# Performance work log

Hardware: AMD Instinct MI355X
Metric: run time of the kernel (lower is better)

The kernel has to match this reference:

```python
import jax, jax.numpy as jnp
import numpy as np
from jax import lax

EPS = 1e-5
C4 = 192   # embed_dim // 4
ED = 768   # embed_dim


def _conv(x, w, stride, pad):
    return lax.conv_general_dilated(x, w, (stride, stride), pad,
                                    dimension_numbers=('NCHW', 'OIHW', 'NCHW'))


def _bn(x, g, b, m, v):
    # inference-mode batchnorm over channel dim (NCHW)
    inv = g * lax.rsqrt(v + EPS)
    return x * inv[None, :, None, None] + (b - m * inv)[None, :, None, None]


def _gelu(x):
    return jax.nn.gelu(x, approximate=False)  # torch nn.GELU default = exact erf


def _region(x, w, g, b, m, v, grid):
    # x: (B,C,H,W); w: (G,C,C,3,3); bn params: (G,C); G = gh*gw
    B, C, H, W = x.shape
    gh, gw = grid
    th, tw = H // gh, W // gw
    tiles = x.reshape(B, C, gh, th, gw, tw).transpose(2, 4, 0, 1, 3, 5)
    tiles = tiles.reshape(gh * gw, B, C, th, tw)

    def per_tile(t, wi, gi, bi, mi, vi):
        y = _gelu(_bn(_conv(t, wi, 1, 'SAME'), gi, bi, mi, vi))
        return y + t  # residual

    out = jax.vmap(per_tile)(tiles, w, g, b, m, v)  # (G,B,C,th,tw)
    out = out.reshape(gh, gw, B, C, th, tw).transpose(2, 3, 0, 4, 1, 5)
    return out.reshape(B, C, H, W)


def _bn_params(key, c):
    k1, k2, k3, k4 = jax.random.split(key, 4)
    return (1.0 + 0.1 * jax.random.normal(k1, (c,)),
            0.1 * jax.random.normal(k2, (c,)),
            0.1 * jax.random.normal(k3, (c,)),
            jax.random.uniform(k4, (c,), minval=0.5, maxval=1.5))


def setup_inputs() -> dict:
    key = jax.random.key(0)
    ks = jax.random.split(key, 12)
    x = jax.random.normal(ks[0], (64, 3, 224, 224), dtype=jnp.float32)
    conv1_w = 0.02 * jax.random.normal(ks[1], (C4, 3, 4, 4))
    bn1_g, bn1_b, bn1_m, bn1_v = _bn_params(ks[2], C4)
    r1_w = 0.02 * jax.random.normal(ks[3], (64, C4, C4, 3, 3))
    r1_g, r1_b, r1_m, r1_v = _bn_params(ks[4], C4)
    r1_g, r1_b, r1_m, r1_v = (jnp.tile(p[None], (64, 1)) * (1.0 + 0.01 * jax.random.normal(jax.random.fold_in(ks[4], i), (64, C4))) for i, p in enumerate((r1_g, r1_b, r1_m, r1_v)))
    conv2_w = 0.02 * jax.random.normal(ks[5], (C4, C4, 2, 2))
    bn2_g, bn2_b, bn2_m, bn2_v = _bn_params(ks[6], C4)
    r2_w = 0.02 * jax.random.normal(ks[7], (16, C4, C4, 3, 3))
    r2_g, r2_b, r2_m, r2_v = _bn_params(ks[8], C4)
    r2_g, r2_b, r2_m, r2_v = (jnp.tile(p[None], (16, 1)) * (1.0 + 0.01 * jax.random.normal(jax.random.fold_in(ks[8], i), (16, C4))) for i, p in enumerate((r2_g, r2_b, r2_m, r2_v)))
    conv3_w = 0.02 * jax.random.normal(ks[9], (ED, C4, 2, 2))
    bn3_g, bn3_b, bn3_m, bn3_v = _bn_params(ks[10], ED)
    return dict(x=x, conv1_w=conv1_w, bn1_g=bn1_g, bn1_b=bn1_b, bn1_m=bn1_m, bn1_v=bn1_v,
                r1_w=r1_w, r1_g=r1_g, r1_b=r1_b, r1_m=r1_m, r1_v=r1_v,
                conv2_w=conv2_w, bn2_g=bn2_g, bn2_b=bn2_b, bn2_m=bn2_m, bn2_v=bn2_v,
                r2_w=r2_w, r2_g=r2_g, r2_b=r2_b, r2_m=r2_m, r2_v=r2_v,
                conv3_w=conv3_w, bn3_g=bn3_g, bn3_b=bn3_b, bn3_m=bn3_m, bn3_v=bn3_v)


def reference(x, conv1_w, bn1_g, bn1_b, bn1_m, bn1_v,
              r1_w, r1_g, r1_b, r1_m, r1_v,
              conv2_w, bn2_g, bn2_b, bn2_m, bn2_v,
              r2_w, r2_g, r2_b, r2_m, r2_v,
              conv3_w, bn3_g, bn3_b, bn3_m, bn3_v):
    h = _gelu(_bn(_conv(x, conv1_w, 4, 'VALID'), bn1_g, bn1_b, bn1_m, bn1_v))   # (B,192,56,56)
    h = _region(h, r1_w, r1_g, r1_b, r1_m, r1_v, (8, 8))
    h = _gelu(_bn(_conv(h, conv2_w, 2, 'VALID'), bn2_g, bn2_b, bn2_m, bn2_v))   # (B,192,28,28)
    h = _region(h, r2_w, r2_g, r2_b, r2_m, r2_v, (4, 4))
    h = _bn(_conv(h, conv3_w, 2, 'VALID'), bn3_g, bn3_b, bn3_m, bn3_v)          # (B,768,14,14)
    B = h.shape[0]
    return h.reshape(B, ED, -1).transpose(0, 2, 1)                               # (B,196,768)
```

## Files before the change

kernel.cpp:

```cpp
#include <hip/hip_runtime.h>
#include <hip/hip_bf16.h>
#include <math.h>

#define EPSBN 1e-5f

typedef short short8 __attribute__((ext_vector_type(8)));
typedef short short4v __attribute__((ext_vector_type(4)));
typedef float floatx4 __attribute__((ext_vector_type(4)));

__device__ __forceinline__ float gelu_f(float x) {
    return 0.5f * x * (1.0f + erff(x * 0.70710678118654752f));
}

__device__ __forceinline__ unsigned short f2bf(float f) {
    union { float f; unsigned int u; } c; c.f = f;
    unsigned int u = c.u;
    unsigned int r = (u + 0x7FFFu + ((u >> 16) & 1u)) >> 16;
    return (unsigned short)r;
}

__device__ __forceinline__ float bf2f(unsigned short h) {
    union { unsigned int u; float f; } c; c.u = ((unsigned int)h) << 16;
    return c.f;
}

__global__ void wprep_bf16_k(const float* __restrict__ w, unsigned short* __restrict__ wb,
                             long total) {
    for (long o = (long)blockIdx.x * blockDim.x + threadIdx.x; o < total;
         o += (long)gridDim.x * blockDim.x) {
        int ic = (int)(o % 192); long t0 = o / 192;
        int t = (int)(t0 % 9); long t1 = t0 / 9;
        int oc = (int)(t1 % 192); long g = t1 / 192;
        wb[o] = f2bf(w[(((size_t)g * 192 + oc) * 192 + ic) * 9 + t]);
    }
}

__global__ void wprep_tap_k(const float* __restrict__ w, unsigned short* __restrict__ wb,
                            int OC) {
    long total = (long)4 * OC * 192;
    for (long o = (long)blockIdx.x * blockDim.x + threadIdx.x; o < total;
         o += (long)gridDim.x * blockDim.x) {
        int ic = (int)(o % 192); long t0 = o / 192;
        int oc = (int)(t0 % OC); int t = (int)(t0 / OC);
        wb[o] = f2bf(w[((size_t)oc * 192 + ic) * 4 + t]);
    }
}

__global__ void wprep_wt1_k(const float* __restrict__ w, float* __restrict__ wt) {
    int o = blockIdx.x * 256 + threadIdx.x;
    if (o < 9216) {
        int oc = o % 192, k = o / 192;
        wt[o] = w[oc * 48 + k];
    }
}

__global__ __launch_bounds__(192) void conv1_k(
        const float* __restrict__ x, const float* __restrict__ wt1,
        const float* __restrict__ bg, const float* __restrict__ bb,
        const float* __restrict__ bm, const float* __restrict__ bv,
        unsigned short* __restrict__ h1c) {
    __shared__ float xs[3][4][224];
    int b = blockIdx.x / 56, oy = blockIdx.x % 56;
    int tid = threadIdx.x;
    for (int i = tid; i < 2688; i += 192) {
        int col = i % 224, r = (i / 224) % 4, c = i / 896;
        xs[c][r][col] = x[(((size_t)b * 3 + c) * 224 + 4 * oy + r) * 224 + col];
    }
    float w[48];
    #pragma unroll
    for (int k = 0; k < 48; k++) w[k] = wt1[k * 192 + tid];
    float inv = bg[tid] * rsqrtf(bv[tid] + EPSBN);
    float bet = bb[tid] - bm[tid] * inv;
    __syncthreads();
    for (int ox = 0; ox < 56; ox++) {
        float a = 0.f;
        #pragma unroll
        for (int c = 0; c < 3; c++) {
            #pragma unroll
            for (int ky = 0; ky < 4; ky++) {
                float4 v = *(const float4*)&xs[c][ky][4 * ox];
                const float* wk = &w[(c * 4 + ky) * 4];
                a += v.x * wk[0] + v.y * wk[1] + v.z * wk[2] + v.w * wk[3];
            }
        }
        h1c[(((size_t)b * 56 + oy) * 56 + ox) * 192 + tid] = f2bf(gelu_f(a * inv + bet));
    }
}

#define RST 200
#define TILE_SH (81 * RST)
template<int INF32>
__global__ __launch_bounds__(256, 2) void region_mfma3_k(
        const void* __restrict__ inbuf, void* __restrict__ outbuf,
        const unsigned short* __restrict__ wb,
        const float* __restrict__ pg, const float* __restrict__ pb,
        const float* __restrict__ pm, const float* __restrict__ pv,
        int gw, int W) {
    __shared__ unsigned short lds[2 * TILE_SH];
    const int raw = blockIdx.x;
    const int g = (raw & 7) + 8 * (raw >> 8);
    const int bp = (raw >> 3) & 31;
    const int b0 = bp * 2;
    const int gy = g / gw, gx = g % gw;
    const int Y0 = gy * 7, X0 = gx * 7;
    const int tid = threadIdx.x;
    const int lane = tid & 63;
    const int wid = tid >> 6;
    const int quad = lane >> 4;
    const int l15 = lane & 15;

    const size_t tsz = (size_t)W * W * 192;
    const size_t slab0 = (size_t)b0 * tsz;

    for (int i = tid; i < 1536; i += 256) {
        int tI = i / 768, rem = i % 768, h = rem / 24, ch = rem % 24;
        int cell;
        if (h < 9) cell = h;
        else if (h < 18) cell = 72 + (h - 9);
        else { int h2 = h - 18; cell = (1 + (h2 >> 1)) * 9 + ((h2 & 1) * 8); }
        *(short8*)&lds[tI * TILE_SH + cell * RST + ch * 8] = (short8)0;
    }
    for (int i = tid; i < 2352; i += 256) {
        int tI = i / 1176, rem = i % 1176, p = rem / 24, ch = rem % 24;
        int y = p / 7, xx = p % 7;
        size_t poff = slab0 + (size_t)tI * tsz + ((size_t)(Y0 + y) * W + (X0 + xx)) * 192 + ch * 8;
        short8 v;
        if (INF32) {
            const float* s4 = (const float*)inbuf + poff;
            float4 a = *(const float4*)s4;
            float4 b2 = *(const float4*)(s4 + 4);
            v[0] = (short)f2bf(a.x);  v[1] = (short)f2bf(a.y);
            v[2] = (short)f2bf(a.z);  v[3] = (short)f2bf(a.w);
            v[4] = (short)f2bf(b2.x); v[5] = (short)f2bf(b2.y);
            v[6] = (short)f2bf(b2.z); v[7] = (short)f2bf(b2.w);
        } else {
            v = *(const short8*)((const unsigned short*)inbuf + poff);
        }
        *(short8*)&lds[tI * TILE_SH + ((y + 1) * 9 + (xx + 1)) * RST + ch * 8] = v;
    }
    __syncthreads();

    int pyv[4], pxv[4];
    #pragma unroll
    for (int f = 0; f < 4; f++) {
        int p = f * 16 + l15; if (p > 48) p = 48;
        pyv[f] = p / 7; pxv[f] = p % 7;
    }
    int woff[3];
    #pragma unroll
    for (int nt = 0; nt < 3; nt++)
        woff[nt] = (wid * 48 + nt * 16 + l15) * 1728 + quad * 8;
    const unsigned short* wbg = wb + (size_t)g * 331776;

    floatx4 acc[8][3];
    #pragma unroll
    for (int m = 0; m < 8; m++)
        #pragma unroll
        for (int nt = 0; nt < 3; nt++) acc[m][nt] = (floatx4)0.f;

    for (int t = 0; t < 9; t++) {
        const int ky = t / 3, kx = t % 3;
        int ca[8];
        #pragma unroll
        for (int f = 0; f < 4; f++) {
            int cell = ((pyv[f] + ky) * 9 + (pxv[f] + kx)) * RST + quad * 8;
            ca[f] = cell;
            ca[4 + f] = TILE_SH + cell;
        }
        const int toff = t * 192;
        #pragma unroll
        for (int s = 0; s < 6; s++) {
            const int ic0 = s * 32;
            short8 wf[3];
            #pragma unroll
            for (int nt = 0; nt < 3; nt++)
                wf[nt] = *(const short8*)(wbg + woff[nt] + toff + ic0);
            short8 pf[8];
            #pragma unroll
            for (int m = 0; m < 8; m++)
                pf[m] = *(const short8*)&lds[ca[m] + ic0];
            #pragma unroll
            for (int m = 0; m < 8; m++)
                #pragma unroll
                for (int nt = 0; nt < 3; nt++)
                    acc[m][nt] = __builtin_amdgcn_mfma_f32_16x16x32_bf16(pf[m], wf[nt], acc[m][nt], 0, 0, 0);
        }
    }

    #pragma unroll
    for (int nt = 0; nt < 3; nt++) {
        int oc = wid * 48 + nt * 16 + l15;
        float inv = pg[g * 192 + oc] * rsqrtf(pv[g * 192 + oc] + EPSBN);
        float bet = pb[g * 192 + oc] - pm[g * 192 + oc] * inv;
        #pragma unroll
        for (int m = 0; m < 8; m++) {
            const int tI = m >> 3 ? 1 : (m >> 2);
            const int f = m & 3;
            const size_t tslab = slab0 + (size_t)tI * tsz;
            unsigned short* outb = (unsigned short*)outbuf + tslab;
            const float* resf = (const float*)inbuf + tslab;
            const unsigned short* resu = (const unsigned short*)inbuf + tslab;
            #pragma unroll
            for (int r = 0; r < 4; r++) {
                int p = f * 16 + quad * 4 + r;
                if (p < 49) {
                    int y = p / 7, xx = p % 7;
                    size_t pix = (size_t)(Y0 + y) * W + (X0 + xx);
                    float res = INF32 ? resf[pix * 192 + oc] : bf2f(resu[pix * 192 + oc]);
                    outb[pix * 192 + oc] = f2bf(gelu_f(acc[m][nt][r] * inv + bet) + res);
                }
            }
        }
    }
}

__global__ __launch_bounds__(256) void conv2_mfma_k(
        const unsigned short* __restrict__ h1c, const unsigned short* __restrict__ wb,
        const float* __restrict__ bg, const float* __restrict__ bb,
        const float* __restrict__ bm, const float* __restrict__ bv,
        float* __restrict__ h2c) {
    __shared__ unsigned short lds[2 * 112 * 40];
    const int b = blockIdx.x / 7;
    const int oy0 = (blockIdx.x % 7) * 4;
    const int tid = threadIdx.x;
    const int lane = tid & 63;
    const int wid = tid >> 6;
    const int quad = lane >> 4;
    const int l15 = lane & 15;

    floatx4 acc[7][3];
    #pragma unroll
    for (int mt = 0; mt < 7; mt++)
        #pragma unroll
        for (int nt = 0; nt < 3; nt++) acc[mt][nt] = (floatx4)0.f;

    for (int ky = 0; ky < 2; ky++) {
        for (int c = 0; c < 6; c++) {
            __syncthreads();
            for (int i = tid; i < 1792; i += 256) {
                int icq = i & 7, kx = (i >> 3) & 1, p = i >> 4;
                int oy = oy0 + p / 28, ox = p % 28;
                int iy = 2 * oy + ky, ix = 2 * ox + kx;
                const unsigned short* src =
                    h1c + (((size_t)b * 56 + iy) * 56 + ix) * 192 + c * 32 + icq * 4;
                *(short4v*)(&lds[kx * 4480 + p * 40 + icq * 4]) = *(const short4v*)src;
            }
            __syncthreads();
            #pragma unroll
            for (int kx = 0; kx < 2; kx++) {
                const int t = ky * 2 + kx;
                short8 wf[3];
                #pragma unroll
                for (int nt = 0; nt < 3; nt++) {
                    int oc = wid * 48 + nt * 16 + l15;
                    wf[nt] = *(const short8*)(wb + ((size_t)(t * 192 + oc)) * 192 + c * 32 + quad * 8);
                }
                #pragma unroll
                for (int mt = 0; mt < 7; mt++) {
                    short8 ap = *(const short8*)(&lds[kx * 4480 + (mt * 16 + l15) * 40 + quad * 8]);
                    #pragma unroll
                    for (int nt = 0; nt < 3; nt++)
                        acc[mt][nt] = __builtin_amdgcn_mfma_f32_16x16x32_bf16(ap, wf[nt], acc[mt][nt], 0, 0, 0);
                }
            }
        }
    }
    #pragma unroll
    for (int nt = 0; nt < 3; nt++) {
        int oc = wid * 48 + nt * 16 + l15;
        float inv = bg[oc] * rsqrtf(bv[oc] + EPSBN);
        float bet = bb[oc] - bm[oc] * inv;
        #pragma unroll
        for (int mt = 0; mt < 7; mt++) {
            #pragma unroll
            for (int r = 0; r < 4; r++) {
                int p = mt * 16 + quad * 4 + r;
                int oy = oy0 + p / 28, ox = p % 28;
                h2c[(((size_t)b * 28 + oy) * 28 + ox) * 192 + oc] = gelu_f(acc[mt][nt][r] * inv + bet);
            }
        }
    }
}

__global__ __launch_bounds__(256) void conv3_mfma_k(
        const unsigned short* __restrict__ h2b, const unsigned short* __restrict__ wb,
        const float* __restrict__ bg, const float* __restrict__ bb,
        const float* __restrict__ bm, const float* __restrict__ bv,
        float* __restrict__ out) {
    __shared__ unsigned short lds[2 * 112 * 40];
    const int bid = blockIdx.x;
    const int b = bid / 6;
    const int s = (bid % 6) / 3;
    const int octile = bid % 3;
    const int y0 = s * 7;
    const int tid = threadIdx.x;
    const int lane = tid & 63;
    const int wid = tid >> 6;
    const int quad = lane >> 4;
    const int l15 = lane & 15;

    floatx4 acc[7][4];
    #pragma unroll
    for (int mt = 0; mt < 7; mt++)
        #pragma unroll
        for (int nt = 0; nt < 4; nt++) acc[mt][nt] = (floatx4)0.f;

    for (int ky = 0; ky < 2; ky++) {
        for (int c = 0; c < 6; c++) {
            __syncthreads();
            for (int i = tid; i < 1568; i += 256) {
                int icq = i & 7, kx = (i >> 3) & 1, p = i >> 4;
                int oy = y0 + p / 14, ox = p % 14;
                int iy = 2 * oy + ky, ix = 2 * ox + kx;
                const unsigned short* src =
                    h2b + (((size_t)b * 28 + iy) * 28 + ix) * 192 + c * 32 + icq * 4;
                *(short4v*)(&lds[kx * 4480 + p * 40 + icq * 4]) = *(const short4v*)src;
            }
            __syncthreads();
            #pragma unroll
            for (int kx = 0; kx < 2; kx++) {
                const int t = ky * 2 + kx;
                short8 wf[4];
                #pragma unroll
                for (int nt = 0; nt < 4; nt++) {
                    int oc = octile * 256 + wid * 64 + nt * 16 + l15;
                    wf[nt] = *(const short8*)(wb + ((size_t)(t * 768 + oc)) * 192 + c * 32 + quad * 8);
                }
                #pragma unroll
                for (int mt = 0; mt < 7; mt++) {
                    int p = mt * 16 + l15; if (p > 97) p = 97;
                    short8 ap = *(const short8*)(&lds[kx * 4480 + p * 40 + quad * 8]);
                    #pragma unroll
                    for (int nt = 0; nt < 4; nt++)
                        acc[mt][nt] = __builtin_amdgcn_mfma_f32_16x16x32_bf16(ap, wf[nt], acc[mt][nt], 0, 0, 0);
                }
            }
        }
    }
    #pragma unroll
    for (int nt = 0; nt < 4; nt++) {
        int oc = octile * 256 + wid * 64 + nt * 16 + l15;
        float inv = bg[oc] * rsqrtf(bv[oc] + EPSBN);
        float bet = bb[oc] - bm[oc] * inv;
        #pragma unroll
        for (int mt = 0; mt < 7; mt++) {
            #pragma unroll
            for (int r = 0; r < 4; r++) {
                int p = mt * 16 + quad * 4 + r;
                if (p < 98) {
                    int oy = y0 + p / 14, ox = p % 14;
                    out[((size_t)b * 196 + oy * 14 + ox) * 768 + oc] = acc[mt][nt][r] * inv + bet;
                }
            }
        }
    }
}

extern "C" void kernel_launch(void* const* d_in, const int* in_sizes, int n_in,
                              void* d_out, int out_size, void* d_ws, size_t ws_size,
                              hipStream_t stream) {
    const float* x   = (const float*)d_in[0];
    const float* w1  = (const float*)d_in[1];
    const float* b1g = (const float*)d_in[2];
    const float* b1b = (const float*)d_in[3];
    const float* b1m = (const float*)d_in[4];
    const float* b1v = (const float*)d_in[5];
    const float* r1w = (const float*)d_in[6];
    const float* r1g = (const float*)d_in[7];
    const float* r1b = (const float*)d_in[8];
    const float* r1m = (const float*)d_in[9];
    const float* r1v = (const float*)d_in[10];
    const float* w2  = (const float*)d_in[11];
    const float* b2g = (const float*)d_in[12];
    const float* b2b = (const float*)d_in[13];
    const float* b2m = (const float*)d_in[14];
    const float* b2v = (const float*)d_in[15];
    const float* r2w = (const float*)d_in[16];
    const float* r2g = (const float*)d_in[17];
    const float* r2b = (const float*)d_in[18];
    const float* r2m = (const float*)d_in[19];
    const float* r2v = (const float*)d_in[20];
    const float* w3  = (const float*)d_in[21];
    const float* b3g = (const float*)d_in[22];
    const float* b3b = (const float*)d_in[23];
    const float* b3m = (const float*)d_in[24];
    const float* b3v = (const float*)d_in[25];
    float* out = (float*)d_out;

    char* ws = (char*)d_ws;
    unsigned short* h1c  = (unsigned short*)(ws + 0);
    float*          h2c  = (float*)         (ws + 77070336UL);
    unsigned short* h2b  = (unsigned short*)(ws + 115605504UL);
    unsigned short* wb1  = (unsigned short*)(ws + 134873088UL);
    unsigned short* wb2r = (unsigned short*)(ws + 177340416UL);
    float*          wt1  = (float*)         (ws + 187957248UL);
    unsigned short* wb2c = (unsigned short*)(ws + 187994112UL);
    unsigned short* wb3c = (unsigned short*)(ws + 188289024UL);

    wprep_bf16_k<<<8192, 256, 0, stream>>>(r1w, wb1, (long)64 * 192 * 9 * 192);
    wprep_bf16_k<<<2048, 256, 0, stream>>>(r2w, wb2r, (long)16 * 192 * 9 * 192);
    wprep_tap_k<<<576, 256, 0, stream>>>(w2, wb2c, 192);
    wprep_tap_k<<<2304, 256, 0, stream>>>(w3, wb3c, 768);
    wprep_wt1_k<<<36, 256, 0, stream>>>(w1, wt1);

    conv1_k<<<64 * 56, 192, 0, stream>>>(x, wt1, b1g, b1b, b1m, b1v, h1c);
    region_mfma3_k<0><<<64 * 32, 256, 0, stream>>>(h1c, h1c, wb1, r1g, r1b, r1m, r1v, 8, 56);
    conv2_mfma_k<<<64 * 7, 256, 0, stream>>>(h1c, wb2c, b2g, b2b, b2m, b2v, h2c);
    region_mfma3_k<1><<<16 * 32, 256, 0, stream>>>(h2c, h2b, wb2r, r2g, r2b, r2m, r2v, 4, 28);
    conv3_mfma_k<<<64 * 6, 256, 0, stream>>>(h2b, wb3c, b3g, b3b, b3m, b3v, out);
}
```

Measured before the change: 867.4 us.

## Split conv1 rows, compact region LDS tile, load conv2/conv3 operands directly

conv1 now launches two blocks per output row, each covering half the columns, which doubles the grid and halves per-block work. The region kernel drops the padded 9x9 halo layout for a compact 7x7 tile plus one zero cell, and maps out-of-range taps to that cell; this shrinks LDS use and the zeroing work. conv2 and conv3 drop their LDS staging and __syncthreads, loading MFMA A-fragments straight from global memory with precomputed pixel offsets and fully unrolled loops. This removes the barriers and staging copies, at the cost of uncoalesced global loads and higher register pressure.

After: 873.3 us. Within noise of the previous version (+0.7%).

```diff
diff --git a/kernel.cpp b/kernel.cpp
--- a/kernel.cpp
+++ b/kernel.cpp
@@ -5,7 +5,6 @@
 #define EPSBN 1e-5f
 
 typedef short short8 __attribute__((ext_vector_type(8)));
-typedef short short4v __attribute__((ext_vector_type(4)));
 typedef float floatx4 __attribute__((ext_vector_type(4)));
 
 __device__ __forceinline__ float gelu_f(float x) {
@@ -59,12 +58,15 @@
         const float* __restrict__ bg, const float* __restrict__ bb,
         const float* __restrict__ bm, const float* __restrict__ bv,
         unsigned short* __restrict__ h1c) {
-    __shared__ float xs[3][4][224];
-    int b = blockIdx.x / 56, oy = blockIdx.x % 56;
+    __shared__ float xs[3][4][112];
+    int b = blockIdx.x / 112;
+    int rest = blockIdx.x % 112;
+    int oy = rest >> 1;
+    int ox0 = (rest & 1) * 28;
     int tid = threadIdx.x;
-    for (int i = tid; i < 2688; i += 192) {
-        int col = i % 224, r = (i / 224) % 4, c = i / 896;
-        xs[c][r][col] = x[(((size_t)b * 3 + c) * 224 + 4 * oy + r) * 224 + col];
+    for (int i = tid; i < 1344; i += 192) {
+        int col = i % 112, r = (i / 112) % 4, c = i / 448;
+        xs[c][r][col] = x[(((size_t)b * 3 + c) * 224 + 4 * oy + r) * 224 + 4 * ox0 + col];
     }
     float w[48];
     #pragma unroll
@@ -72,7 +74,7 @@
     float inv = bg[tid] * rsqrtf(bv[tid] + EPSBN);
     float bet = bb[tid] - bm[tid] * inv;
     __syncthreads();
-    for (int ox = 0; ox < 56; ox++) {
+    for (int ox = 0; ox < 28; ox++) {
         float a = 0.f;
         #pragma unroll
         for (int c = 0; c < 3; c++) {
@@ -83,14 +85,15 @@
                 a += v.x * wk[0] + v.y * wk[1] + v.z * wk[2] + v.w * wk[3];
             }
         }
-        h1c[(((size_t)b * 56 + oy) * 56 + ox) * 192 + tid] = f2bf(gelu_f(a * inv + bet));
+        h1c[(((size_t)b * 56 + oy) * 56 + (ox0 + ox)) * 192 + tid] = f2bf(gelu_f(a * inv + bet));
     }
 }
 
 #define RST 200
-#define TILE_SH (81 * RST)
+#define NCELL 50
+#define TILE_SH (NCELL * RST)
 template<int INF32>
-__global__ __launch_bounds__(256, 2) void region_mfma3_k(
+__global__ __launch_bounds__(256, 2) void region_mfma4_k(
         const void* __restrict__ inbuf, void* __restrict__ outbuf,
         const unsigned short* __restrict__ wb,
         const float* __restrict__ pg, const float* __restrict__ pb,
@@ -112,13 +115,9 @@
     const size_t tsz = (size_t)W * W * 192;
     const size_t slab0 = (size_t)b0 * tsz;
 
-    for (int i = tid; i < 1536; i += 256) {
-        int tI = i / 768, rem = i % 768, h = rem / 24, ch = rem % 24;
-        int cell;
-        if (h < 9) cell = h;
-        else if (h < 18) cell = 72 + (h - 9);
-        else { int h2 = h - 18; cell = (1 + (h2 >> 1)) * 9 + ((h2 & 1) * 8); }
-        *(short8*)&lds[tI * TILE_SH + cell * RST + ch * 8] = (short8)0;
+    for (int i = tid; i < 48; i += 256) {
+        int tI = i / 24, ch = i % 24;
+        *(short8*)&lds[tI * TILE_SH + 49 * RST + ch * 8] = (short8)0;
     }
     for (int i = tid; i < 2352; i += 256) {
         int tI = i / 1176, rem = i % 1176, p = rem / 24, ch = rem % 24;
@@ -136,7 +135,7 @@
         } else {
             v = *(const short8*)((const unsigned short*)inbuf + poff);
         }
-        *(short8*)&lds[tI * TILE_SH + ((y + 1) * 9 + (xx + 1)) * RST + ch * 8] = v;
+        *(short8*)&lds[tI * TILE_SH + p * RST + ch * 8] = v;
     }
     __syncthreads();
 
@@ -158,14 +157,17 @@
         #pragma unroll
         for (int nt = 0; nt < 3; nt++) acc[m][nt] = (floatx4)0.f;
 
+    #pragma unroll
     for (int t = 0; t < 9; t++) {
-        const int ky = t / 3, kx = t % 3;
+        const int dy = t / 3 - 1, dx = t % 3 - 1;
         int ca[8];
         #pragma unroll
         for (int f = 0; f < 4; f++) {
-            int cell = ((pyv[f] + ky) * 9 + (pxv[f] + kx)) * RST + quad * 8;
-            ca[f] = cell;
-            ca[4 + f] = TILE_SH + cell;
+            int yy = pyv[f] + dy, xx2 = pxv[f] + dx;
+            bool ok = ((unsigned)yy < 7u) & ((unsigned)xx2 < 7u);
+            int cell = ok ? (yy * 7 + xx2) : 49;
+            ca[f] = cell * RST + quad * 8;
+            ca[4 + f] = TILE_SH + ca[f];
         }
         const int toff = t * 192;
         #pragma unroll
@@ -194,7 +196,7 @@
         float bet = pb[g * 192 + oc] - pm[g * 192 + oc] * inv;
         #pragma unroll
         for (int m = 0; m < 8; m++) {
-            const int tI = m >> 3 ? 1 : (m >> 2);
+            const int tI = m >> 2;
             const int f = m & 3;
             const size_t tslab = slab0 + (size_t)tI * tsz;
             unsigned short* outb = (unsigned short*)outbuf + tslab;
@@ -219,7 +221,6 @@
         const float* __restrict__ bg, const float* __restrict__ bb,
         const float* __restrict__ bm, const float* __restrict__ bv,
         float* __restrict__ h2c) {
-    __shared__ unsigned short lds[2 * 112 * 40];
     const int b = blockIdx.x / 7;
     const int oy0 = (blockIdx.x % 7) * 4;
     const int tid = threadIdx.x;
@@ -228,40 +229,43 @@
     const int quad = lane >> 4;
     const int l15 = lane & 15;
 
+    size_t pixoff[7];
+    #pragma unroll
+    for (int mt = 0; mt < 7; mt++) {
+        int p = mt * 16 + l15;
+        int oy = oy0 + p / 28, ox = p % 28;
+        pixoff[mt] = (((size_t)b * 56 + 2 * oy) * 56 + 2 * ox) * 192 + quad * 8;
+    }
+
     floatx4 acc[7][3];
     #pragma unroll
     for (int mt = 0; mt < 7; mt++)
         #pragma unroll
         for (int nt = 0; nt < 3; nt++) acc[mt][nt] = (floatx4)0.f;
 
+    #pragma unroll
     for (int ky = 0; ky < 2; ky++) {
-        for (int c = 0; c < 6; c++) {
-            __syncthreads();
-            for (int i = tid; i < 1792; i += 256) {
-                int icq = i & 7, kx = (i >> 3) & 1, p = i >> 4;
-                int oy = oy0 + p / 28, ox = p % 28;
-                int iy = 2 * oy + ky, ix = 2 * ox + kx;
-                const unsigned short* src =
-                    h1c + (((size_t)b * 56 + iy) * 56 + ix) * 192 + c * 32 + icq * 4;
-                *(short4v*)(&lds[kx * 4480 + p * 40 + icq * 4]) = *(const short4v*)src;
-            }
-            __syncthreads();
-            #pragma unroll
-            for (int kx = 0; kx < 2; kx++) {
-                const int t = ky * 2 + kx;
+        #pragma unroll
+        for (int kx = 0; kx < 2; kx++) {
+            const int t = ky * 2 + kx;
+            const size_t aoff = ((size_t)ky * 56 + kx) * 192;
+            #pragma unroll
+            for (int c = 0; c < 6; c++) {
                 short8 wf[3];
                 #pragma unroll
                 for (int nt = 0; nt < 3; nt++) {
                     int oc = wid * 48 + nt * 16 + l15;
                     wf[nt] = *(const short8*)(wb + ((size_t)(t * 192 + oc)) * 192 + c * 32 + quad * 8);
                 }
-                #pragma unroll
-                for (int mt = 0; mt < 7; mt++) {
-                    short8 ap = *(const short8*)(&lds[kx * 4480 + (mt * 16 + l15) * 40 + quad * 8]);
+                short8 ap[7];
+                #pragma unroll
+                for (int mt = 0; mt < 7; mt++)
+                    ap[mt] = *(const short8*)(h1c + pixoff[mt] + aoff + c * 32);
+                #pragma unroll
+                for (int mt = 0; mt < 7; mt++)
                     #pragma unroll
                     for (int nt = 0; nt < 3; nt++)
-                        acc[mt][nt] = __builtin_amdgcn_mfma_f32_16x16x32_bf16(ap, wf[nt], acc[mt][nt], 0, 0, 0);
-                }
+                        acc[mt][nt] = __builtin_amdgcn_mfma_f32_16x16x32_bf16(ap[mt], wf[nt], acc[mt][nt], 0, 0, 0);
             }
         }
     }
@@ -287,7 +291,6 @@
         const float* __restrict__ bg, const float* __restrict__ bb,
         const float* __restrict__ bm, const float* __restrict__ bv,
         float* __restrict__ out) {
-    __shared__ unsigned short lds[2 * 112 * 40];
     const int bid = blockIdx.x;
     const int b = bid / 6;
     const int s = (bid % 6) / 3;
@@ -299,41 +302,43 @@
     const int quad = lane >> 4;
     const int l15 = lane & 15;
 
+    size_t pixoff[7];
+    #pragma unroll
+    for (int mt = 0; mt < 7; mt++) {
+        int p = mt * 16 + l15; if (p > 97) p = 97;
+        int oy = y0 + p / 14, ox = p % 14;
+        pixoff[mt] = (((size_t)b * 28 + 2 * oy) * 28 + 2 * ox) * 192 + quad * 8;
+    }
+
     floatx4 acc[7][4];
     #pragma unroll
     for (int mt = 0; mt < 7; mt++)
         #pragma unroll
         for (int nt = 0; nt < 4; nt++) acc[mt][nt] = (floatx4)0.f;
 
+    #pragma unroll
     for (int ky = 0; ky < 2; ky++) {
-        for (int c = 0; c < 6; c++) {
-            __syncthreads();
-            for (int i = tid; i < 1568; i += 256) {
-                int icq = i & 7, kx = (i >> 3) & 1, p = i >> 4;
-                int oy = y0 + p / 14, ox = p % 14;
-                int iy = 2 * oy + ky, ix = 2 * ox + kx;
-                const unsigned short* src =
-                    h2b + (((size_t)b * 28 + iy) * 28 + ix) * 192 + c * 32 + icq * 4;
-                *(short4v*)(&lds[kx * 4480 + p * 40 + icq * 4]) = *(const short4v*)src;
-            }
-            __syncthreads();
-            #pragma unroll
-            for (int kx = 0; kx < 2; kx++) {
-                const int t = ky * 2 + kx;
+        #pragma unroll
+        for (int kx = 0; kx < 2; kx++) {
+            const int t = ky * 2 + kx;
+            const size_t aoff = ((size_t)ky * 28 + kx) * 192;
+            #pragma unroll
+            for (int c = 0; c < 6; c++) {
                 short8 wf[4];
                 #pragma unroll
                 for (int nt = 0; nt < 4; nt++) {
                     int oc = octile * 256 + wid * 64 + nt * 16 + l15;
                     wf[nt] = *(const short8*)(wb + ((size_t)(t * 768 + oc)) * 192 + c * 32 + quad * 8);
                 }
-                #pragma unroll
-                for (int mt = 0; mt < 7; mt++) {
-                    int p = mt * 16 + l15; if (p > 97) p = 97;
-                    short8 ap = *(const short8*)(&lds[kx * 4480 + p * 40 + quad * 8]);
+                short8 ap[7];
+                #pragma unroll
+                for (int mt = 0; mt < 7; mt++)
+                    ap[mt] = *(const short8*)(h2b + pixoff[mt] + aoff + c * 32);
+                #pragma unroll
+                for (int mt = 0; mt < 7; mt++)
                     #pragma unroll
                     for (int nt = 0; nt < 4; nt++)
-                        acc[mt][nt] = __builtin_amdgcn_mfma_f32_16x16x32_bf16(ap, wf[nt], acc[mt][nt], 0, 0, 0);
-                }
+                        acc[mt][nt] = __builtin_amdgcn_mfma_f32_16x16x32_bf16(ap[mt], wf[nt], acc[mt][nt], 0, 0, 0);
             }
         }
     }
@@ -403,9 +408,9 @@
     wprep_tap_k<<<2304, 256, 0, stream>>>(w3, wb3c, 768);
     wprep_wt1_k<<<36, 256, 0, stream>>>(w1, wt1);
 
-    conv1_k<<<64 * 56, 192, 0, stream>>>(x, wt1, b1g, b1b, b1m, b1v, h1c);
-    region_mfma3_k<0><<<64 * 32, 256, 0, stream>>>(h1c, h1c, wb1, r1g, r1b, r1m, r1v, 8, 56);
+    conv1_k<<<64 * 112, 192, 0, stream>>>(x, wt1, b1g, b1b, b1m, b1v, h1c);
+    region_mfma4_k<0><<<64 * 32, 256, 0, stream>>>(h1c, h1c, wb1, r1g, r1b, r1m, r1v, 8, 56);
     conv2_mfma_k<<<64 * 7, 256, 0, stream>>>(h1c, wb2c, b2g, b2b, b2m, b2v, h2c);
-    region_mfma3_k<1><<<16 * 32, 256, 0, stream>>>(h2c, h2b, wb2r, r2g, r2b, r2m, r2v, 4, 28);
+    region_mfma4_k<1><<<16 * 32, 256, 0, stream>>>(h2c, h2b, wb2r, r2g, r2b, r2m, r2v, 4, 28);
     conv3_mfma_k<<<64 * 6, 256, 0, stream>>>(h2b, wb3c, b3g, b3b, b3m, b3v, out);
 }
```
